# Kernel optimization log

Measured on AMD Instinct MI355X. Metric: run time of the kernel, lower is better.

Reference implementation:

```python
import jax, jax.numpy as jnp
import numpy as np

N = 100000   # nodes
E = 1600000  # directed edges (avg degree 16)
H = 64       # MODEL_HIDDEN_CHANNELS


def setup_inputs() -> dict:
    key = jax.random.key(0)
    ks = jax.random.split(key, 6)
    x = jax.random.normal(ks[0], (N, 1), dtype=jnp.float32)
    edge_index = jax.random.randint(ks[1], (2, E), 0, N, dtype=jnp.int32)
    w1 = jax.random.normal(ks[2], (1, H), dtype=jnp.float32) * 0.5
    b1 = jnp.zeros((H,), dtype=jnp.float32)
    w2 = jax.random.normal(ks[3], (H, H), dtype=jnp.float32) * (1.0 / np.sqrt(H))
    b2 = jnp.zeros((H,), dtype=jnp.float32)
    wfc = jax.random.normal(ks[4], (H, 1), dtype=jnp.float32) * (1.0 / np.sqrt(H))
    bfc = jnp.zeros((1,), dtype=jnp.float32)
    return {"x": x, "edge_index": edge_index, "w1": w1, "b1": b1,
            "w2": w2, "b2": b2, "wfc": wfc, "bfc": bfc}


def _gcn_conv(x, src, dst, norm, W, b, n):
    # PyG GCNConv: h = x @ W, then scatter-add of norm-weighted messages at dst, + bias
    h = x @ W                                   # [n, out]
    msg = h[src] * norm[:, None]                # gather + scale, [e, out]
    agg = jax.ops.segment_sum(msg, dst, num_segments=n)
    return agg + b


def reference(x, edge_index, w1, b1, w2, b2, wfc, bfc):
    n = x.shape[0]
    # add self-loops (PyG GCNConv default)
    loops = jnp.arange(n, dtype=edge_index.dtype)
    src = jnp.concatenate([edge_index[0], loops])
    dst = jnp.concatenate([edge_index[1], loops])
    # symmetric degree normalization D^{-1/2} A_hat D^{-1/2}
    deg = jax.ops.segment_sum(jnp.ones(src.shape[0], dtype=x.dtype), dst, num_segments=n)
    dinv = jnp.where(deg > 0, jax.lax.rsqrt(deg), 0.0)
    norm = dinv[src] * dinv[dst]
    h = jax.nn.relu(_gcn_conv(x, src, dst, norm, w1, b1, n))
    h = jax.nn.relu(_gcn_conv(h, src, dst, norm, w2, b2, n))
    out = h @ wfc + bfc                         # [n, 1]
    return out.reshape(-1)
```

## Files before the change

kernel.cpp:

```cpp
#include <hip/hip_runtime.h>


#define HCH 64
#define CHUNK 4096
#define BSH 7
#define BSZ 128
#define NBMAX 1024

__device__ __forceinline__ void lds_addf(float* p, float v) {
    __hip_atomic_fetch_add(p, v, __ATOMIC_RELAXED, __HIP_MEMORY_SCOPE_WORKGROUP);
}

__global__ __launch_bounds__(512) void k_init(int nb, int cap,
                                              int* __restrict__ cursor,
                                              int* __restrict__ ov_cursor,
                                              const float* __restrict__ w1,
                                              const float* __restrict__ b1,
                                              const float* __restrict__ w2,
                                              float* __restrict__ P) {
    __shared__ float part[8][4][HCH];
    __shared__ float sPo[4 * HCH];
    __shared__ float fsum;
    int t = threadIdx.x;
    for (int i = t; i < nb; i += 512) cursor[i] = i * cap;
    if (t == 0) { *ov_cursor = 0; fsum = 0.f; }
    int j = t & 63, seg = t >> 6;
    float pp = 0.f, pm = 0.f, bp = 0.f, bm = 0.f;
#pragma unroll
    for (int kk = 0; kk < 8; kk++) {
        int k = seg * 8 + kk;
        float w = w1[k], b = b1[k], v = w2[k * HCH + j];
        if (w > 0.f) { pp += w * v; bp += b * v; }
        else if (w < 0.f) { pm += w * v; bm += b * v; }
        else { float rb = b > 0.f ? b : 0.f; bp += rb * v; bm += rb * v; }
    }
    part[seg][0][j] = pp; part[seg][1][j] = pm;
    part[seg][2][j] = bp; part[seg][3][j] = bm;
    __syncthreads();
    if (t < 4 * HCH) {
        int c = t >> 6, jj = t & 63;
        float s = 0.f;
#pragma unroll
        for (int g = 0; g < 8; g++) s += part[g][c][jj];
        sPo[t] = s;
        P[t] = s;
        if (c >= 2) lds_addf(&fsum, fabsf(s));
    }
    __syncthreads();
    if (t == 0) P[4 * HCH] = fsum;
}

__global__ __launch_bounds__(512) void k_place(const int* __restrict__ src,
                                               const int* __restrict__ dst, int e,
                                               int nb, int cap,
                                               int* __restrict__ cursor,
                                               int* __restrict__ ov_cursor,
                                               int* __restrict__ packed,
                                               int2* __restrict__ ovbuf) {
    __shared__ int h[NBMAX];
    __shared__ int basel[NBMAX];
    __shared__ int avail[NBMAX];
    __shared__ int lpv[CHUNK];
    __shared__ short lb[CHUNK];
    int t = threadIdx.x;
    for (int i = t; i < nb; i += 512) h[i] = 0;
    __syncthreads();
    int cbase = blockIdx.x * CHUNK;
    int rem = min(e - cbase, CHUNK);
#pragma unroll
    for (int g = 0; g < 2; g++) {
        int li = t * 8 + g * 4;
        if (li + 3 < rem) {
            int4 s4 = *(const int4*)(src + cbase + li);
            int4 d4 = *(const int4*)(dst + cbase + li);
#pragma unroll
            for (int q = 0; q < 4; q++) {
                int sv = (q == 0) ? s4.x : (q == 1) ? s4.y : (q == 2) ? s4.z : s4.w;
                int dv = (q == 0) ? d4.x : (q == 1) ? d4.y : (q == 2) ? d4.z : d4.w;
                int b = dv >> BSH;
                atomicAdd(&h[b], 1);
                lpv[li + q] = sv | ((dv & (BSZ - 1)) << 17);
                lb[li + q] = (short)b;
            }
        } else {
            for (int q = li; q < rem && q < li + 4; q++) {
                int sv = src[cbase + q], dv = dst[cbase + q];
                int b = dv >> BSH;
                atomicAdd(&h[b], 1);
                lpv[q] = sv | ((dv & (BSZ - 1)) << 17);
                lb[q] = (short)b;
            }
        }
    }
    __syncthreads();
    for (int i = t; i < nb; i += 512) {
        int my = h[i];
        int av = 0, base = 0;
        if (my) {
            base = atomicAdd(&cursor[i], my);
            int room = (i + 1) * cap - base;
            av = room < 0 ? 0 : (room > my ? my : room);
        }
        basel[i] = base;
        avail[i] = av;
        h[i] = 0;
    }
    __syncthreads();
    for (int li = t * 8; li < t * 8 + 8 && li < rem; li++) {
        int b = lb[li];
        int pv = lpv[li];
        int loc = atomicAdd(&h[b], 1);
        if (loc < avail[b]) {
            packed[basel[b] + loc] = pv;
        } else {
            int op = atomicAdd(ov_cursor, 1);
            ovbuf[op] = make_int2(pv & 0x1FFFF, (b << BSH) | (pv >> 17));
        }
    }
}

__global__ __launch_bounds__(512) void k_bdeg(const int* __restrict__ packed,
                                              const int* __restrict__ cursor,
                                              const int* __restrict__ ov_cursor,
                                              const int2* __restrict__ ovbuf,
                                              int cap, const float* __restrict__ x, int n,
                                              float* __restrict__ dinv,
                                              float* __restrict__ y) {
    __shared__ int cnt[BSZ];
    int bk = blockIdx.x, t = threadIdx.x;
    int bbase = bk * cap;
    int bcnt = min(cursor[bk] - bbase, cap);
    if (t < BSZ) cnt[t] = 0;
    __syncthreads();
    for (int base = 0; base < bcnt; base += 2048) {
        int i0 = base + t * 4;
        if (i0 + 3 < bcnt) {
            int4 p = *(const int4*)(packed + bbase + i0);
            atomicAdd(&cnt[p.x >> 17], 1);
            atomicAdd(&cnt[p.y >> 17], 1);
            atomicAdd(&cnt[p.z >> 17], 1);
            atomicAdd(&cnt[p.w >> 17], 1);
        } else {
            for (int i = i0; i < bcnt && i < i0 + 4; i++)
                atomicAdd(&cnt[packed[bbase + i] >> 17], 1);
        }
    }
    int ovc = *ov_cursor;
    for (int i = t; i < ovc; i += 512) {
        int2 o = ovbuf[i];
        if ((o.y >> BSH) == bk) atomicAdd(&cnt[o.y & (BSZ - 1)], 1);
    }
    __syncthreads();
    int node = (bk << BSH) + t;
    if (t < BSZ && node < n) {
        float dv = rsqrtf((float)(cnt[t] + 1));
        dinv[node] = dv;
        y[node] = dv * x[node];
    }
}

__global__ __launch_bounds__(512) void k_bagg1(const int* __restrict__ packed,
                                               const int* __restrict__ cursor,
                                               const int* __restrict__ ov_cursor,
                                               const int2* __restrict__ ovbuf,
                                               int cap, const float* __restrict__ x,
                                               const float* __restrict__ dinv,
                                               const float* __restrict__ y, int n,
                                               float2* __restrict__ val2) {
    __shared__ float acc[BSZ];
    int bk = blockIdx.x, t = threadIdx.x;
    int bbase = bk * cap;
    int bcnt = min(cursor[bk] - bbase, cap);
    if (t < BSZ) acc[t] = 0.f;
    __syncthreads();
    for (int base = 0; base < bcnt; base += 2048) {
        int i0 = base + t * 4;
        if (i0 + 3 < bcnt) {
            int4 p = *(const int4*)(packed + bbase + i0);
            float y0 = y[p.x & 0x1FFFF], y1 = y[p.y & 0x1FFFF];
            float y2 = y[p.z & 0x1FFFF], y3 = y[p.w & 0x1FFFF];
            lds_addf(&acc[p.x >> 17], y0);
            lds_addf(&acc[p.y >> 17], y1);
            lds_addf(&acc[p.z >> 17], y2);
            lds_addf(&acc[p.w >> 17], y3);
        } else {
            for (int i = i0; i < bcnt && i < i0 + 4; i++) {
                int p = packed[bbase + i];
                lds_addf(&acc[p >> 17], y[p & 0x1FFFF]);
            }
        }
    }
    int ovc = *ov_cursor;
    for (int i = t; i < ovc; i += 512) {
        int2 o = ovbuf[i];
        if ((o.y >> BSH) == bk) lds_addf(&acc[o.y & (BSZ - 1)], y[o.x]);
    }
    __syncthreads();
    int node = (bk << BSH) + t;
    if (t < BSZ && node < n) {
        float dv = dinv[node];
        float s = dv * (acc[t] + dv * x[node]);
        val2[node] = make_float2(dv * s, dv);
    }
}

__global__ __launch_bounds__(512) void k_bagg2(const int* __restrict__ packed,
                                               const int* __restrict__ cursor,
                                               const int* __restrict__ ov_cursor,
                                               const int2* __restrict__ ovbuf,
                                               int cap, const float2* __restrict__ val2,
                                               const float* __restrict__ dinv,
                                               const float* __restrict__ P,
                                               const float* __restrict__ b2,
                                               const float* __restrict__ wfc,
                                               const float* __restrict__ bfc,
                                               float* __restrict__ out, int n) {
    __shared__ float aa[2 * BSZ];
    __shared__ float cc[2 * BSZ];
    __shared__ float sP[4 * HCH], sb2[HCH], swfc[HCH];
    __shared__ float sflag;
    int bk = blockIdx.x, t = threadIdx.x;
    int bbase = bk * cap;
    int bcnt = min(cursor[bk] - bbase, cap);
    if (t < 2 * BSZ) { aa[t] = 0.f; cc[t] = 0.f; }
    if (t < 4 * HCH) sP[t] = P[t];
    if (t >= 256 && t < 320) sb2[t - 256] = b2[t - 256];
    if (t >= 320 && t < 384) swfc[t - 320] = wfc[t - 320];
    if (t == 448) sflag = P[4 * HCH];
    __syncthreads();
    bool useB = sflag != 0.f;
    for (int base = 0; base < bcnt; base += 2048) {
        int i0 = base + t * 4;
        if (i0 + 3 < bcnt) {
            int4 p = *(const int4*)(packed + bbase + i0);
            float2 v0 = val2[p.x & 0x1FFFF], v1 = val2[p.y & 0x1FFFF];
            float2 v2 = val2[p.z & 0x1FFFF], v3 = val2[p.w & 0x1FFFF];
            int o0 = (v0.x > 0.f ? 0 : BSZ) + (p.x >> 17);
            int o1 = (v1.x > 0.f ? 0 : BSZ) + (p.y >> 17);
            int o2 = (v2.x > 0.f ? 0 : BSZ) + (p.z >> 17);
            int o3 = (v3.x > 0.f ? 0 : BSZ) + (p.w >> 17);
            lds_addf(&aa[o0], v0.x); lds_addf(&aa[o1], v1.x);
            lds_addf(&aa[o2], v2.x); lds_addf(&aa[o3], v3.x);
            if (useB) {
                lds_addf(&cc[o0], v0.y); lds_addf(&cc[o1], v1.y);
                lds_addf(&cc[o2], v2.y); lds_addf(&cc[o3], v3.y);
            }
        } else {
            for (int i = i0; i < bcnt && i < i0 + 4; i++) {
                int p = packed[bbase + i];
                float2 v = val2[p & 0x1FFFF];
                int off = (v.x > 0.f ? 0 : BSZ) + (p >> 17);
                lds_addf(&aa[off], v.x);
                if (useB) lds_addf(&cc[off], v.y);
            }
        }
    }
    int ovc = *ov_cursor;
    for (int i = t; i < ovc; i += 512) {
        int2 o = ovbuf[i];
        if ((o.y >> BSH) == bk) {
            float2 v = val2[o.x];
            int off = (v.x > 0.f ? 0 : BSZ) + (o.y & (BSZ - 1));
            lds_addf(&aa[off], v.x);
            if (useB) lds_addf(&cc[off], v.y);
        }
    }
    __syncthreads();
    int node = (bk << BSH) + t;
    if (t >= BSZ || node >= n) return;
    float a_p = aa[t], a_m = aa[BSZ + t], c_p = cc[t], c_m = cc[BSZ + t];
    float2 sv = val2[node];
    if (sv.x > 0.f) { a_p += sv.x; c_p += sv.y; }
    else            { a_m += sv.x; c_m += sv.y; }
    float dv = dinv[node];
    float acc = 0.f;
#pragma unroll 8
    for (int j = 0; j < HCH; j++) {
        float z = dv * (a_p * sP[j] + a_m * sP[HCH + j] +
                        c_p * sP[2 * HCH + j] + c_m * sP[3 * HCH + j]) + sb2[j];
        z = z > 0.f ? z : 0.f;
        acc += z * swfc[j];
    }
    out[node] = acc + bfc[0];
}

extern "C" void kernel_launch(void* const* d_in, const int* in_sizes, int n_in,
                              void* d_out, int out_size, void* d_ws, size_t ws_size,
                              hipStream_t stream) {
    const float* x   = (const float*)d_in[0];
    const int*   ei  = (const int*)d_in[1];
    const float* w1  = (const float*)d_in[2];
    const float* b1  = (const float*)d_in[3];
    const float* w2  = (const float*)d_in[4];
    const float* b2  = (const float*)d_in[5];
    const float* wfc = (const float*)d_in[6];
    const float* bfc = (const float*)d_in[7];
    float* out = (float*)d_out;

    const int n = in_sizes[0];
    const int e = in_sizes[1] / 2;
    const int* src = ei;
    const int* dst = ei + e;

    const int nb = (n + BSZ - 1) >> BSH;
    int avg = (e + nb - 1) / nb;
    int cap = ((avg + avg / 4 + 64) + 15) & ~15;

    auto al = [](size_t v) { return (v + 255) & ~(size_t)255; };
    char* ws = (char*)d_ws;
    size_t o = 0;
    int* cursor    = (int*)(ws + o);  o = al(o + (size_t)NBMAX * 4);
    int* ov_cursor = (int*)(ws + o);  o = al(o + 256);
    float* dinv  = (float*)(ws + o);  o = al(o + (size_t)n * 4);
    float* y     = (float*)(ws + o);  o = al(o + (size_t)n * 4);
    float2* val2 = (float2*)(ws + o); o = al(o + (size_t)n * 8);
    float* P     = (float*)(ws + o);  o = al(o + (4 * HCH + 8) * 4);
    int* packed  = (int*)(ws + o);    o = al(o + (size_t)nb * cap * 4);
    int2* ovbuf  = (int2*)(ws + o);   o = al(o + (size_t)e * 8);
    (void)ws_size;

    const int nchunk = (e + CHUNK - 1) / CHUNK;

    k_init<<<1, 512, 0, stream>>>(nb, cap, cursor, ov_cursor, w1, b1, w2, P);
    k_place<<<nchunk, 512, 0, stream>>>(src, dst, e, nb, cap, cursor, ov_cursor,
                                        packed, ovbuf);
    k_bdeg<<<nb, 512, 0, stream>>>(packed, cursor, ov_cursor, ovbuf, cap, x, n, dinv, y);
    k_bagg1<<<nb, 512, 0, stream>>>(packed, cursor, ov_cursor, ovbuf, cap, x, dinv, y,
                                    n, val2);
    k_bagg2<<<nb, 512, 0, stream>>>(packed, cursor, ov_cursor, ovbuf, cap, val2, dinv,
                                    P, b2, wfc, bfc, out, n);
}
```

Baseline: 134.5 us.

## Fuse GCN pipeline into one cooperative kernel with grid syncs and larger buckets

Replaces the five separate launches (init, place, degree, aggregation 1, aggregation 2) with a single cooperative kernel that separates phases with grid-wide syncs. Cursor, overflow counter and P are zeroed by a memset, and P is computed inside the degree phase. Bucket size grows from 128 to 256 nodes, which halves the bucket count and gives each block more edges. The aim is to remove per-launch overhead and tail gaps between kernels. In exchange it adds grid.sync costs, caps the grid at what can be co-resident (391 blocks of 512 threads), and uses a larger shared-memory union that may limit occupancy.

```diff
diff --git a/kernel.cpp b/kernel.cpp
--- a/kernel.cpp
+++ b/kernel.cpp
@@ -1,274 +1,244 @@
 #include <hip/hip_runtime.h>
+#include <hip/hip_cooperative_groups.h>
+
+namespace cg = cooperative_groups;
 
 
 #define HCH 64
 #define CHUNK 4096
-#define BSH 7
-#define BSZ 128
-#define NBMAX 1024
+#define BSH 8
+#define BSZ 256
+#define NBMAX 512
 
 __device__ __forceinline__ void lds_addf(float* p, float v) {
     __hip_atomic_fetch_add(p, v, __ATOMIC_RELAXED, __HIP_MEMORY_SCOPE_WORKGROUP);
 }
 
-__global__ __launch_bounds__(512) void k_init(int nb, int cap,
-                                              int* __restrict__ cursor,
-                                              int* __restrict__ ov_cursor,
-                                              const float* __restrict__ w1,
-                                              const float* __restrict__ b1,
-                                              const float* __restrict__ w2,
-                                              float* __restrict__ P) {
-    __shared__ float part[8][4][HCH];
-    __shared__ float sPo[4 * HCH];
-    __shared__ float fsum;
+union SMem {
+    struct { int h[NBMAX]; int basel[NBMAX]; int avail[NBMAX];
+             int lpv[CHUNK]; short lb[CHUNK]; } pl;
+    struct { int cnt[BSZ]; } bd;
+    struct { float acc[BSZ]; } g1;
+    struct { float aa[2 * BSZ]; float cc[2 * BSZ];
+             float sP[4 * HCH]; float sb2[HCH]; float swfc[HCH]; } g2;
+};
+
+__global__ __launch_bounds__(512, 4) void k_fused(
+    const int* __restrict__ src, const int* __restrict__ dst, int e, int n,
+    int nb, int nchunk, int cap,
+    int* __restrict__ cursor, int* __restrict__ ov_cursor,
+    int2* __restrict__ ovbuf, int* __restrict__ packed,
+    const float* __restrict__ x, float* __restrict__ dinv,
+    float* __restrict__ y, float2* __restrict__ val2,
+    const float* __restrict__ w1, const float* __restrict__ b1,
+    const float* __restrict__ w2, float* __restrict__ P,
+    const float* __restrict__ b2v, const float* __restrict__ wfc,
+    const float* __restrict__ bfc, float* __restrict__ out) {
+    __shared__ SMem sm;
+    cg::grid_group grid = cg::this_grid();
     int t = threadIdx.x;
-    for (int i = t; i < nb; i += 512) cursor[i] = i * cap;
-    if (t == 0) { *ov_cursor = 0; fsum = 0.f; }
-    int j = t & 63, seg = t >> 6;
-    float pp = 0.f, pm = 0.f, bp = 0.f, bm = 0.f;
+    int bid = blockIdx.x;
+
+    if (bid < nchunk) {
+        for (int i = t; i < nb; i += 512) sm.pl.h[i] = 0;
+        __syncthreads();
+        int cbase = bid * CHUNK;
+        int rem = min(e - cbase, CHUNK);
 #pragma unroll
-    for (int kk = 0; kk < 8; kk++) {
-        int k = seg * 8 + kk;
-        float w = w1[k], b = b1[k], v = w2[k * HCH + j];
-        if (w > 0.f) { pp += w * v; bp += b * v; }
-        else if (w < 0.f) { pm += w * v; bm += b * v; }
-        else { float rb = b > 0.f ? b : 0.f; bp += rb * v; bm += rb * v; }
-    }
-    part[seg][0][j] = pp; part[seg][1][j] = pm;
-    part[seg][2][j] = bp; part[seg][3][j] = bm;
+        for (int g = 0; g < 2; g++) {
+            int li = t * 8 + g * 4;
+            if (li + 3 < rem) {
+                int4 s4 = *(const int4*)(src + cbase + li);
+                int4 d4 = *(const int4*)(dst + cbase + li);
+#pragma unroll
+                for (int q = 0; q < 4; q++) {
+                    int sv = (q == 0) ? s4.x : (q == 1) ? s4.y : (q == 2) ? s4.z : s4.w;
+                    int dv = (q == 0) ? d4.x : (q == 1) ? d4.y : (q == 2) ? d4.z : d4.w;
+                    int b = dv >> BSH;
+                    atomicAdd(&sm.pl.h[b], 1);
+                    sm.pl.lpv[li + q] = sv | ((dv & (BSZ - 1)) << 17);
+                    sm.pl.lb[li + q] = (short)b;
+                }
+            } else {
+                for (int q = li; q < rem && q < li + 4; q++) {
+                    int sv = src[cbase + q], dv = dst[cbase + q];
+                    int b = dv >> BSH;
+                    atomicAdd(&sm.pl.h[b], 1);
+                    sm.pl.lpv[q] = sv | ((dv & (BSZ - 1)) << 17);
+                    sm.pl.lb[q] = (short)b;
+                }
+            }
+        }
+        __syncthreads();
+        for (int i = t; i < nb; i += 512) {
+            int my = sm.pl.h[i];
+            int av = 0, base = 0;
+            if (my) {
+                base = atomicAdd(&cursor[i], my);
+                int room = cap - base;
+                av = room < 0 ? 0 : (room > my ? my : room);
+            }
+            sm.pl.basel[i] = i * cap + base;
+            sm.pl.avail[i] = av;
+            sm.pl.h[i] = 0;
+        }
+        __syncthreads();
+        int lim = min(rem, t * 8 + 8);
+        for (int li = t * 8; li < lim; li++) {
+            int b = sm.pl.lb[li];
+            int pv = sm.pl.lpv[li];
+            int loc = atomicAdd(&sm.pl.h[b], 1);
+            if (loc < sm.pl.avail[b]) {
+                packed[sm.pl.basel[b] + loc] = pv;
+            } else {
+                int op = atomicAdd(ov_cursor, 1);
+                ovbuf[op] = make_int2(pv & 0x1FFFF, (b << BSH) | (pv >> 17));
+            }
+        }
+    }
+    grid.sync();
+
+    if (bid < nb) {
+        if (t < BSZ) sm.bd.cnt[t] = 0;
+        __syncthreads();
+        int bbase = bid * cap;
+        int bcnt = min(cursor[bid], cap);
+        for (int base = 0; base < bcnt; base += 2048) {
+            int i0 = base + t * 4;
+            if (i0 + 3 < bcnt) {
+                int4 p = *(const int4*)(packed + bbase + i0);
+                atomicAdd(&sm.bd.cnt[p.x >> 17], 1);
+                atomicAdd(&sm.bd.cnt[p.y >> 17], 1);
+                atomicAdd(&sm.bd.cnt[p.z >> 17], 1);
+                atomicAdd(&sm.bd.cnt[p.w >> 17], 1);
+            } else {
+                for (int i = i0; i < bcnt && i < i0 + 4; i++)
+                    atomicAdd(&sm.bd.cnt[packed[bbase + i] >> 17], 1);
+            }
+        }
+        int ovc = *ov_cursor;
+        for (int i = t; i < ovc; i += 512) {
+            int2 o = ovbuf[i];
+            if ((o.y >> BSH) == bid) atomicAdd(&sm.bd.cnt[o.y & (BSZ - 1)], 1);
+        }
+        __syncthreads();
+        int node = (bid << BSH) + t;
+        if (t < BSZ && node < n) {
+            float dv = rsqrtf((float)(sm.bd.cnt[t] + 1));
+            dinv[node] = dv;
+            y[node] = dv * x[node];
+        }
+    }
+    if (bid == 0 && t < 4 * HCH) {
+        int c = t >> 6, j = t & 63;
+        float acc = 0.f;
+        for (int k = 0; k < HCH; k++) {
+            float w = w1[k], b = b1[k], v = w2[k * HCH + j];
+            if (c == 0)      acc += (w > 0.f) ? w * v : 0.f;
+            else if (c == 1) acc += (w < 0.f) ? w * v : 0.f;
+            else if (c == 2) acc += (w > 0.f) ? b * v : (w == 0.f ? fmaxf(b, 0.f) * v : 0.f);
+            else             acc += (w < 0.f) ? b * v : (w == 0.f ? fmaxf(b, 0.f) * v : 0.f);
+        }
+        P[t] = acc;
+        if (c >= 2) {
+            float f = fabsf(acc);
+#pragma unroll
+            for (int off = 32; off; off >>= 1) f += __shfl_xor(f, off, 64);
+            if ((t & 63) == 0) atomicAdd(&P[4 * HCH], f);
+        }
+    }
+    grid.sync();
+
+    if (bid < nb) {
+        if (t < BSZ) sm.g1.acc[t] = 0.f;
+        __syncthreads();
+        int bbase = bid * cap;
+        int bcnt = min(cursor[bid], cap);
+        for (int base = 0; base < bcnt; base += 2048) {
+            int i0 = base + t * 4;
+            if (i0 + 3 < bcnt) {
+                int4 p = *(const int4*)(packed + bbase + i0);
+                float y0 = y[p.x & 0x1FFFF], y1 = y[p.y & 0x1FFFF];
+                float y2 = y[p.z & 0x1FFFF], y3 = y[p.w & 0x1FFFF];
+                lds_addf(&sm.g1.acc[p.x >> 17], y0);
+                lds_addf(&sm.g1.acc[p.y >> 17], y1);
+                lds_addf(&sm.g1.acc[p.z >> 17], y2);
+                lds_addf(&sm.g1.acc[p.w >> 17], y3);
+            } else {
+                for (int i = i0; i < bcnt && i < i0 + 4; i++) {
+                    int p = packed[bbase + i];
+                    lds_addf(&sm.g1.acc[p >> 17], y[p & 0x1FFFF]);
+                }
+            }
+        }
+        int ovc = *ov_cursor;
+        for (int i = t; i < ovc; i += 512) {
+            int2 o = ovbuf[i];
+            if ((o.y >> BSH) == bid) lds_addf(&sm.g1.acc[o.y & (BSZ - 1)], y[o.x]);
+        }
+        __syncthreads();
+        int node = (bid << BSH) + t;
+        if (t < BSZ && node < n) {
+            float dv = dinv[node];
+            float s = dv * (sm.g1.acc[t] + dv * x[node]);
+            val2[node] = make_float2(dv * s, dv);
+        }
+    }
+    grid.sync();
+
+    if (bid >= nb) return;
+    sm.g2.aa[t] = 0.f;
+    sm.g2.cc[t] = 0.f;
+    if (t < 4 * HCH) sm.g2.sP[t] = P[t];
+    if (t >= 256 && t < 320) sm.g2.sb2[t - 256] = b2v[t - 256];
+    if (t >= 320 && t < 384) sm.g2.swfc[t - 320] = wfc[t - 320];
     __syncthreads();
-    if (t < 4 * HCH) {
-        int c = t >> 6, jj = t & 63;
-        float s = 0.f;
-#pragma unroll
-        for (int g = 0; g < 8; g++) s += part[g][c][jj];
-        sPo[t] = s;
-        P[t] = s;
-        if (c >= 2) lds_addf(&fsum, fabsf(s));
+    bool useB = P[4 * HCH] != 0.f;
+    {
+        int bbase = bid * cap;
+        int bcnt = min(cursor[bid], cap);
+        for (int base = 0; base < bcnt; base += 2048) {
+            int i0 = base + t * 4;
+            if (i0 + 3 < bcnt) {
+                int4 p = *(const int4*)(packed + bbase + i0);
+                float2 v0 = val2[p.x & 0x1FFFF], v1 = val2[p.y & 0x1FFFF];
+                float2 v2 = val2[p.z & 0x1FFFF], v3 = val2[p.w & 0x1FFFF];
+                int o0 = (v0.x > 0.f ? 0 : BSZ) + (p.x >> 17);
+                int o1 = (v1.x > 0.f ? 0 : BSZ) + (p.y >> 17);
+                int o2 = (v2.x > 0.f ? 0 : BSZ) + (p.z >> 17);
+                int o3 = (v3.x > 0.f ? 0 : BSZ) + (p.w >> 17);
+                lds_addf(&sm.g2.aa[o0], v0.x); lds_addf(&sm.g2.aa[o1], v1.x);
+                lds_addf(&sm.g2.aa[o2], v2.x); lds_addf(&sm.g2.aa[o3], v3.x);
+                if (useB) {
+                    lds_addf(&sm.g2.cc[o0], v0.y); lds_addf(&sm.g2.cc[o1], v1.y);
+                    lds_addf(&sm.g2.cc[o2], v2.y); lds_addf(&sm.g2.cc[o3], v3.y);
+                }
+            } else {
+                for (int i = i0; i < bcnt && i < i0 + 4; i++) {
+                    int p = packed[bbase + i];
+                    float2 v = val2[p & 0x1FFFF];
+                    int off = (v.x > 0.f ? 0 : BSZ) + (p >> 17);
+                    lds_addf(&sm.g2.aa[off], v.x);
+                    if (useB) lds_addf(&sm.g2.cc[off], v.y);
+                }
+            }
+        }
+        int ovc = *ov_cursor;
+        for (int i = t; i < ovc; i += 512) {
+            int2 o = ovbuf[i];
+            if ((o.y >> BSH) == bid) {
+                float2 v = val2[o.x];
+                int off = (v.x > 0.f ? 0 : BSZ) + (o.y & (BSZ - 1));
+                lds_addf(&sm.g2.aa[off], v.x);
+                if (useB) lds_addf(&sm.g2.cc[off], v.y);
+            }
+        }
     }
     __syncthreads();
-    if (t == 0) P[4 * HCH] = fsum;
-}
-
-__global__ __launch_bounds__(512) void k_place(const int* __restrict__ src,
-                                               const int* __restrict__ dst, int e,
-                                               int nb, int cap,
-                                               int* __restrict__ cursor,
-                                               int* __restrict__ ov_cursor,
-                                               int* __restrict__ packed,
-                                               int2* __restrict__ ovbuf) {
-    __shared__ int h[NBMAX];
-    __shared__ int basel[NBMAX];
-    __shared__ int avail[NBMAX];
-    __shared__ int lpv[CHUNK];
-    __shared__ short lb[CHUNK];
-    int t = threadIdx.x;
-    for (int i = t; i < nb; i += 512) h[i] = 0;
-    __syncthreads();
-    int cbase = blockIdx.x * CHUNK;
-    int rem = min(e - cbase, CHUNK);
-#pragma unroll
-    for (int g = 0; g < 2; g++) {
-        int li = t * 8 + g * 4;
-        if (li + 3 < rem) {
-            int4 s4 = *(const int4*)(src + cbase + li);
-            int4 d4 = *(const int4*)(dst + cbase + li);
-#pragma unroll
-            for (int q = 0; q < 4; q++) {
-                int sv = (q == 0) ? s4.x : (q == 1) ? s4.y : (q == 2) ? s4.z : s4.w;
-                int dv = (q == 0) ? d4.x : (q == 1) ? d4.y : (q == 2) ? d4.z : d4.w;
-                int b = dv >> BSH;
-                atomicAdd(&h[b], 1);
-                lpv[li + q] = sv | ((dv & (BSZ - 1)) << 17);
-                lb[li + q] = (short)b;
-            }
-        } else {
-            for (int q = li; q < rem && q < li + 4; q++) {
-                int sv = src[cbase + q], dv = dst[cbase + q];
-                int b = dv >> BSH;
-                atomicAdd(&h[b], 1);
-                lpv[q] = sv | ((dv & (BSZ - 1)) << 17);
-                lb[q] = (short)b;
-            }
-        }
-    }
-    __syncthreads();
-    for (int i = t; i < nb; i += 512) {
-        int my = h[i];
-        int av = 0, base = 0;
-        if (my) {
-            base = atomicAdd(&cursor[i], my);
-            int room = (i + 1) * cap - base;
-            av = room < 0 ? 0 : (room > my ? my : room);
-        }
-        basel[i] = base;
-        avail[i] = av;
-        h[i] = 0;
-    }
-    __syncthreads();
-    for (int li = t * 8; li < t * 8 + 8 && li < rem; li++) {
-        int b = lb[li];
-        int pv = lpv[li];
-        int loc = atomicAdd(&h[b], 1);
-        if (loc < avail[b]) {
-            packed[basel[b] + loc] = pv;
-        } else {
-            int op = atomicAdd(ov_cursor, 1);
-            ovbuf[op] = make_int2(pv & 0x1FFFF, (b << BSH) | (pv >> 17));
-        }
-    }
-}
-
-__global__ __launch_bounds__(512) void k_bdeg(const int* __restrict__ packed,
-                                              const int* __restrict__ cursor,
-                                              const int* __restrict__ ov_cursor,
-                                              const int2* __restrict__ ovbuf,
-                                              int cap, const float* __restrict__ x, int n,
-                                              float* __restrict__ dinv,
-                                              float* __restrict__ y) {
-    __shared__ int cnt[BSZ];
-    int bk = blockIdx.x, t = threadIdx.x;
-    int bbase = bk * cap;
-    int bcnt = min(cursor[bk] - bbase, cap);
-    if (t < BSZ) cnt[t] = 0;
-    __syncthreads();
-    for (int base = 0; base < bcnt; base += 2048) {
-        int i0 = base + t * 4;
-        if (i0 + 3 < bcnt) {
-            int4 p = *(const int4*)(packed + bbase + i0);
-            atomicAdd(&cnt[p.x >> 17], 1);
-            atomicAdd(&cnt[p.y >> 17], 1);
-            atomicAdd(&cnt[p.z >> 17], 1);
-            atomicAdd(&cnt[p.w >> 17], 1);
-        } else {
-            for (int i = i0; i < bcnt && i < i0 + 4; i++)
-                atomicAdd(&cnt[packed[bbase + i] >> 17], 1);
-        }
-    }
-    int ovc = *ov_cursor;
-    for (int i = t; i < ovc; i += 512) {
-        int2 o = ovbuf[i];
-        if ((o.y >> BSH) == bk) atomicAdd(&cnt[o.y & (BSZ - 1)], 1);
-    }
-    __syncthreads();
-    int node = (bk << BSH) + t;
-    if (t < BSZ && node < n) {
-        float dv = rsqrtf((float)(cnt[t] + 1));
-        dinv[node] = dv;
-        y[node] = dv * x[node];
-    }
-}
-
-__global__ __launch_bounds__(512) void k_bagg1(const int* __restrict__ packed,
-                                               const int* __restrict__ cursor,
-                                               const int* __restrict__ ov_cursor,
-                                               const int2* __restrict__ ovbuf,
-                                               int cap, const float* __restrict__ x,
-                                               const float* __restrict__ dinv,
-                                               const float* __restrict__ y, int n,
-                                               float2* __restrict__ val2) {
-    __shared__ float acc[BSZ];
-    int bk = blockIdx.x, t = threadIdx.x;
-    int bbase = bk * cap;
-    int bcnt = min(cursor[bk] - bbase, cap);
-    if (t < BSZ) acc[t] = 0.f;
-    __syncthreads();
-    for (int base = 0; base < bcnt; base += 2048) {
-        int i0 = base + t * 4;
-        if (i0 + 3 < bcnt) {
-            int4 p = *(const int4*)(packed + bbase + i0);
-            float y0 = y[p.x & 0x1FFFF], y1 = y[p.y & 0x1FFFF];
-            float y2 = y[p.z & 0x1FFFF], y3 = y[p.w & 0x1FFFF];
-            lds_addf(&acc[p.x >> 17], y0);
-            lds_addf(&acc[p.y >> 17], y1);
-            lds_addf(&acc[p.z >> 17], y2);
-            lds_addf(&acc[p.w >> 17], y3);
-        } else {
-            for (int i = i0; i < bcnt && i < i0 + 4; i++) {
-                int p = packed[bbase + i];
-                lds_addf(&acc[p >> 17], y[p & 0x1FFFF]);
-            }
-        }
-    }
-    int ovc = *ov_cursor;
-    for (int i = t; i < ovc; i += 512) {
-        int2 o = ovbuf[i];
-        if ((o.y >> BSH) == bk) lds_addf(&acc[o.y & (BSZ - 1)], y[o.x]);
-    }
-    __syncthreads();
-    int node = (bk << BSH) + t;
-    if (t < BSZ && node < n) {
-        float dv = dinv[node];
-        float s = dv * (acc[t] + dv * x[node]);
-        val2[node] = make_float2(dv * s, dv);
-    }
-}
-
-__global__ __launch_bounds__(512) void k_bagg2(const int* __restrict__ packed,
-                                               const int* __restrict__ cursor,
-                                               const int* __restrict__ ov_cursor,
-                                               const int2* __restrict__ ovbuf,
-                                               int cap, const float2* __restrict__ val2,
-                                               const float* __restrict__ dinv,
-                                               const float* __restrict__ P,
-                                               const float* __restrict__ b2,
-                                               const float* __restrict__ wfc,
-                                               const float* __restrict__ bfc,
-                                               float* __restrict__ out, int n) {
-    __shared__ float aa[2 * BSZ];
-    __shared__ float cc[2 * BSZ];
-    __shared__ float sP[4 * HCH], sb2[HCH], swfc[HCH];
-    __shared__ float sflag;
-    int bk = blockIdx.x, t = threadIdx.x;
-    int bbase = bk * cap;
-    int bcnt = min(cursor[bk] - bbase, cap);
-    if (t < 2 * BSZ) { aa[t] = 0.f; cc[t] = 0.f; }
-    if (t < 4 * HCH) sP[t] = P[t];
-    if (t >= 256 && t < 320) sb2[t - 256] = b2[t - 256];
-    if (t >= 320 && t < 384) swfc[t - 320] = wfc[t - 320];
-    if (t == 448) sflag = P[4 * HCH];
-    __syncthreads();
-    bool useB = sflag != 0.f;
-    for (int base = 0; base < bcnt; base += 2048) {
-        int i0 = base + t * 4;
-        if (i0 + 3 < bcnt) {
-            int4 p = *(const int4*)(packed + bbase + i0);
-            float2 v0 = val2[p.x & 0x1FFFF], v1 = val2[p.y & 0x1FFFF];
-            float2 v2 = val2[p.z & 0x1FFFF], v3 = val2[p.w & 0x1FFFF];
-            int o0 = (v0.x > 0.f ? 0 : BSZ) + (p.x >> 17);
-            int o1 = (v1.x > 0.f ? 0 : BSZ) + (p.y >> 17);
-            int o2 = (v2.x > 0.f ? 0 : BSZ) + (p.z >> 17);
-            int o3 = (v3.x > 0.f ? 0 : BSZ) + (p.w >> 17);
-            lds_addf(&aa[o0], v0.x); lds_addf(&aa[o1], v1.x);
-            lds_addf(&aa[o2], v2.x); lds_addf(&aa[o3], v3.x);
-            if (useB) {
-                lds_addf(&cc[o0], v0.y); lds_addf(&cc[o1], v1.y);
-                lds_addf(&cc[o2], v2.y); lds_addf(&cc[o3], v3.y);
-            }
-        } else {
-            for (int i = i0; i < bcnt && i < i0 + 4; i++) {
-                int p = packed[bbase + i];
-                float2 v = val2[p & 0x1FFFF];
-                int off = (v.x > 0.f ? 0 : BSZ) + (p >> 17);
-                lds_addf(&aa[off], v.x);
-                if (useB) lds_addf(&cc[off], v.y);
-            }
-        }
-    }
-    int ovc = *ov_cursor;
-    for (int i = t; i < ovc; i += 512) {
-        int2 o = ovbuf[i];
-        if ((o.y >> BSH) == bk) {
-            float2 v = val2[o.x];
-            int off = (v.x > 0.f ? 0 : BSZ) + (o.y & (BSZ - 1));
-            lds_addf(&aa[off], v.x);
-            if (useB) lds_addf(&cc[off], v.y);
-        }
-    }
-    __syncthreads();
-    int node = (bk << BSH) + t;
+    int node = (bid << BSH) + t;
     if (t >= BSZ || node >= n) return;
-    float a_p = aa[t], a_m = aa[BSZ + t], c_p = cc[t], c_m = cc[BSZ + t];
+    float a_p = sm.g2.aa[t], a_m = sm.g2.aa[BSZ + t];
+    float c_p = sm.g2.cc[t], c_m = sm.g2.cc[BSZ + t];
     float2 sv = val2[node];
     if (sv.x > 0.f) { a_p += sv.x; c_p += sv.y; }
     else            { a_m += sv.x; c_m += sv.y; }
@@ -276,10 +246,11 @@
     float acc = 0.f;
 #pragma unroll 8
     for (int j = 0; j < HCH; j++) {
-        float z = dv * (a_p * sP[j] + a_m * sP[HCH + j] +
-                        c_p * sP[2 * HCH + j] + c_m * sP[3 * HCH + j]) + sb2[j];
-        z = z > 0.f ? z : 0.f;
-        acc += z * swfc[j];
+        float z = dv * (a_p * sm.g2.sP[j] + a_m * sm.g2.sP[HCH + j] +
+                        c_p * sm.g2.sP[2 * HCH + j] + c_m * sm.g2.sP[3 * HCH + j]) +
+                  sm.g2.sb2[j];
+        z = fmaxf(z, 0.f);
+        acc += z * sm.g2.swfc[j];
     }
     out[node] = acc + bfc[0];
 }
@@ -297,36 +268,37 @@
     const float* bfc = (const float*)d_in[7];
     float* out = (float*)d_out;
 
-    const int n = in_sizes[0];
-    const int e = in_sizes[1] / 2;
+    int n = in_sizes[0];
+    int e = in_sizes[1] / 2;
     const int* src = ei;
     const int* dst = ei + e;
 
-    const int nb = (n + BSZ - 1) >> BSH;
+    int nb = (n + BSZ - 1) >> BSH;
+    int nchunk = (e + CHUNK - 1) / CHUNK;
     int avg = (e + nb - 1) / nb;
     int cap = ((avg + avg / 4 + 64) + 15) & ~15;
 
     auto al = [](size_t v) { return (v + 255) & ~(size_t)255; };
     char* ws = (char*)d_ws;
     size_t o = 0;
-    int* cursor    = (int*)(ws + o);  o = al(o + (size_t)NBMAX * 4);
-    int* ov_cursor = (int*)(ws + o);  o = al(o + 256);
+    int* cursor    = (int*)(ws + o);  o += (size_t)NBMAX * 4;
+    int* ov_cursor = (int*)(ws + o);  o += 256;
+    float* P       = (float*)(ws + o); o += (4 * HCH + 8) * 4;
+    size_t zbytes = o;
+    o = al(o);
     float* dinv  = (float*)(ws + o);  o = al(o + (size_t)n * 4);
     float* y     = (float*)(ws + o);  o = al(o + (size_t)n * 4);
     float2* val2 = (float2*)(ws + o); o = al(o + (size_t)n * 8);
-    float* P     = (float*)(ws + o);  o = al(o + (4 * HCH + 8) * 4);
     int* packed  = (int*)(ws + o);    o = al(o + (size_t)nb * cap * 4);
     int2* ovbuf  = (int2*)(ws + o);   o = al(o + (size_t)e * 8);
     (void)ws_size;
 
-    const int nchunk = (e + CHUNK - 1) / CHUNK;
-
-    k_init<<<1, 512, 0, stream>>>(nb, cap, cursor, ov_cursor, w1, b1, w2, P);
-    k_place<<<nchunk, 512, 0, stream>>>(src, dst, e, nb, cap, cursor, ov_cursor,
-                                        packed, ovbuf);
-    k_bdeg<<<nb, 512, 0, stream>>>(packed, cursor, ov_cursor, ovbuf, cap, x, n, dinv, y);
-    k_bagg1<<<nb, 512, 0, stream>>>(packed, cursor, ov_cursor, ovbuf, cap, x, dinv, y,
-                                    n, val2);
-    k_bagg2<<<nb, 512, 0, stream>>>(packed, cursor, ov_cursor, ovbuf, cap, val2, dinv,
-                                    P, b2, wfc, bfc, out, n);
+    int grid = nb > nchunk ? nb : nchunk;
+
+    hipMemsetAsync(ws, 0, zbytes, stream);
+    void* args[] = {&src, &dst, &e, &n, &nb, &nchunk, &cap,
+                    &cursor, &ov_cursor, &ovbuf, &packed,
+                    &x, &dinv, &y, &val2,
+                    &w1, &b1, &w2, &P, &b2, &wfc, &bfc, &out};
+    hipLaunchCooperativeKernel((void*)k_fused, dim3(grid), dim3(512), args, 0, stream);
 }
```

New measurement: 313.1 us. 2.33x slower.

## Drop init kernel: memset cursors, fold weight precompute into degree kernel

Applied to the files above, without the earlier changes.

Removes the single-block init kernel. Cursors, the overflow counter and P are now zeroed with one hipMemsetAsync, and cursors hold offsets relative to each bucket instead of absolute positions. The W1·W2 split precompute moves into block 0 of the degree kernel, which uses a wave shuffle reduction and a global atomic for the bias-magnitude flag. The placement kernel also switches to 1024 threads with 4 edges per thread. Together these remove one dependent launch from the chain, at the cost of a memset node and extra serial work in one block of k_bdeg.

```diff
diff --git a/kernel.cpp b/kernel.cpp
--- a/kernel.cpp
+++ b/kernel.cpp
@@ -11,104 +11,63 @@
     __hip_atomic_fetch_add(p, v, __ATOMIC_RELAXED, __HIP_MEMORY_SCOPE_WORKGROUP);
 }
 
-__global__ __launch_bounds__(512) void k_init(int nb, int cap,
-                                              int* __restrict__ cursor,
-                                              int* __restrict__ ov_cursor,
-                                              const float* __restrict__ w1,
-                                              const float* __restrict__ b1,
-                                              const float* __restrict__ w2,
-                                              float* __restrict__ P) {
-    __shared__ float part[8][4][HCH];
-    __shared__ float sPo[4 * HCH];
-    __shared__ float fsum;
-    int t = threadIdx.x;
-    for (int i = t; i < nb; i += 512) cursor[i] = i * cap;
-    if (t == 0) { *ov_cursor = 0; fsum = 0.f; }
-    int j = t & 63, seg = t >> 6;
-    float pp = 0.f, pm = 0.f, bp = 0.f, bm = 0.f;
-#pragma unroll
-    for (int kk = 0; kk < 8; kk++) {
-        int k = seg * 8 + kk;
-        float w = w1[k], b = b1[k], v = w2[k * HCH + j];
-        if (w > 0.f) { pp += w * v; bp += b * v; }
-        else if (w < 0.f) { pm += w * v; bm += b * v; }
-        else { float rb = b > 0.f ? b : 0.f; bp += rb * v; bm += rb * v; }
-    }
-    part[seg][0][j] = pp; part[seg][1][j] = pm;
-    part[seg][2][j] = bp; part[seg][3][j] = bm;
-    __syncthreads();
-    if (t < 4 * HCH) {
-        int c = t >> 6, jj = t & 63;
-        float s = 0.f;
-#pragma unroll
-        for (int g = 0; g < 8; g++) s += part[g][c][jj];
-        sPo[t] = s;
-        P[t] = s;
-        if (c >= 2) lds_addf(&fsum, fabsf(s));
-    }
-    __syncthreads();
-    if (t == 0) P[4 * HCH] = fsum;
-}
-
-__global__ __launch_bounds__(512) void k_place(const int* __restrict__ src,
-                                               const int* __restrict__ dst, int e,
-                                               int nb, int cap,
-                                               int* __restrict__ cursor,
-                                               int* __restrict__ ov_cursor,
-                                               int* __restrict__ packed,
-                                               int2* __restrict__ ovbuf) {
+__global__ __launch_bounds__(1024) void k_place(const int* __restrict__ src,
+                                                const int* __restrict__ dst, int e,
+                                                int nb, int cap,
+                                                int* __restrict__ cursor,
+                                                int* __restrict__ ov_cursor,
+                                                int* __restrict__ packed,
+                                                int2* __restrict__ ovbuf) {
     __shared__ int h[NBMAX];
     __shared__ int basel[NBMAX];
     __shared__ int avail[NBMAX];
     __shared__ int lpv[CHUNK];
     __shared__ short lb[CHUNK];
     int t = threadIdx.x;
-    for (int i = t; i < nb; i += 512) h[i] = 0;
+    if (t < nb) h[t] = 0;
     __syncthreads();
     int cbase = blockIdx.x * CHUNK;
     int rem = min(e - cbase, CHUNK);
+    int li = t * 4;
+    if (li + 3 < rem) {
+        int4 s4 = *(const int4*)(src + cbase + li);
+        int4 d4 = *(const int4*)(dst + cbase + li);
 #pragma unroll
-    for (int g = 0; g < 2; g++) {
-        int li = t * 8 + g * 4;
-        if (li + 3 < rem) {
-            int4 s4 = *(const int4*)(src + cbase + li);
-            int4 d4 = *(const int4*)(dst + cbase + li);
-#pragma unroll
-            for (int q = 0; q < 4; q++) {
-                int sv = (q == 0) ? s4.x : (q == 1) ? s4.y : (q == 2) ? s4.z : s4.w;
-                int dv = (q == 0) ? d4.x : (q == 1) ? d4.y : (q == 2) ? d4.z : d4.w;
-                int b = dv >> BSH;
-                atomicAdd(&h[b], 1);
-                lpv[li + q] = sv | ((dv & (BSZ - 1)) << 17);
-                lb[li + q] = (short)b;
-            }
-        } else {
-            for (int q = li; q < rem && q < li + 4; q++) {
-                int sv = src[cbase + q], dv = dst[cbase + q];
-                int b = dv >> BSH;
-                atomicAdd(&h[b], 1);
-                lpv[q] = sv | ((dv & (BSZ - 1)) << 17);
-                lb[q] = (short)b;
-            }
-        }
-    }
-    __syncthreads();
-    for (int i = t; i < nb; i += 512) {
-        int my = h[i];
+        for (int q = 0; q < 4; q++) {
+            int sv = (q == 0) ? s4.x : (q == 1) ? s4.y : (q == 2) ? s4.z : s4.w;
+            int dv = (q == 0) ? d4.x : (q == 1) ? d4.y : (q == 2) ? d4.z : d4.w;
+            int b = dv >> BSH;
+            atomicAdd(&h[b], 1);
+            lpv[li + q] = sv | ((dv & (BSZ - 1)) << 17);
+            lb[li + q] = (short)b;
+        }
+    } else {
+        for (int q = li; q < rem && q < li + 4; q++) {
+            int sv = src[cbase + q], dv = dst[cbase + q];
+            int b = dv >> BSH;
+            atomicAdd(&h[b], 1);
+            lpv[q] = sv | ((dv & (BSZ - 1)) << 17);
+            lb[q] = (short)b;
+        }
+    }
+    __syncthreads();
+    if (t < nb) {
+        int my = h[t];
         int av = 0, base = 0;
         if (my) {
-            base = atomicAdd(&cursor[i], my);
-            int room = (i + 1) * cap - base;
+            base = atomicAdd(&cursor[t], my);
+            int room = cap - base;
             av = room < 0 ? 0 : (room > my ? my : room);
         }
-        basel[i] = base;
-        avail[i] = av;
-        h[i] = 0;
-    }
-    __syncthreads();
-    for (int li = t * 8; li < t * 8 + 8 && li < rem; li++) {
-        int b = lb[li];
-        int pv = lpv[li];
+        basel[t] = t * cap + base;
+        avail[t] = av;
+        h[t] = 0;
+    }
+    __syncthreads();
+    int lim = min(rem, li + 4);
+    for (int q = li; q < lim; q++) {
+        int b = lb[q];
+        int pv = lpv[q];
         int loc = atomicAdd(&h[b], 1);
         if (loc < avail[b]) {
             packed[basel[b] + loc] = pv;
@@ -125,11 +84,15 @@
                                               const int2* __restrict__ ovbuf,
                                               int cap, const float* __restrict__ x, int n,
                                               float* __restrict__ dinv,
-                                              float* __restrict__ y) {
+                                              float* __restrict__ y,
+                                              const float* __restrict__ w1,
+                                              const float* __restrict__ b1,
+                                              const float* __restrict__ w2,
+                                              float* __restrict__ P) {
     __shared__ int cnt[BSZ];
     int bk = blockIdx.x, t = threadIdx.x;
     int bbase = bk * cap;
-    int bcnt = min(cursor[bk] - bbase, cap);
+    int bcnt = min(cursor[bk], cap);
     if (t < BSZ) cnt[t] = 0;
     __syncthreads();
     for (int base = 0; base < bcnt; base += 2048) {
@@ -157,6 +120,25 @@
         dinv[node] = dv;
         y[node] = dv * x[node];
     }
+    if (bk == 0 && t >= 128 && t < 384) {
+        int tt = t - 128;
+        int c = tt >> 6, j = tt & 63;
+        float acc = 0.f;
+        for (int k = 0; k < HCH; k++) {
+            float w = w1[k], b = b1[k], v = w2[k * HCH + j];
+            if (c == 0)      acc += (w > 0.f) ? w * v : 0.f;
+            else if (c == 1) acc += (w < 0.f) ? w * v : 0.f;
+            else if (c == 2) acc += (w > 0.f) ? b * v : (w == 0.f ? fmaxf(b, 0.f) * v : 0.f);
+            else             acc += (w < 0.f) ? b * v : (w == 0.f ? fmaxf(b, 0.f) * v : 0.f);
+        }
+        P[c * HCH + j] = acc;
+        if (c >= 2) {
+            float f = fabsf(acc);
+#pragma unroll
+            for (int off = 32; off; off >>= 1) f += __shfl_xor(f, off, 64);
+            if ((t & 63) == 0) atomicAdd(&P[4 * HCH], f);
+        }
+    }
 }
 
 __global__ __launch_bounds__(512) void k_bagg1(const int* __restrict__ packed,
@@ -170,7 +152,7 @@
     __shared__ float acc[BSZ];
     int bk = blockIdx.x, t = threadIdx.x;
     int bbase = bk * cap;
-    int bcnt = min(cursor[bk] - bbase, cap);
+    int bcnt = min(cursor[bk], cap);
     if (t < BSZ) acc[t] = 0.f;
     __syncthreads();
     for (int base = 0; base < bcnt; base += 2048) {
@@ -218,17 +200,15 @@
     __shared__ float aa[2 * BSZ];
     __shared__ float cc[2 * BSZ];
     __shared__ float sP[4 * HCH], sb2[HCH], swfc[HCH];
-    __shared__ float sflag;
     int bk = blockIdx.x, t = threadIdx.x;
     int bbase = bk * cap;
-    int bcnt = min(cursor[bk] - bbase, cap);
+    int bcnt = min(cursor[bk], cap);
     if (t < 2 * BSZ) { aa[t] = 0.f; cc[t] = 0.f; }
     if (t < 4 * HCH) sP[t] = P[t];
     if (t >= 256 && t < 320) sb2[t - 256] = b2[t - 256];
     if (t >= 320 && t < 384) swfc[t - 320] = wfc[t - 320];
-    if (t == 448) sflag = P[4 * HCH];
-    __syncthreads();
-    bool useB = sflag != 0.f;
+    __syncthreads();
+    bool useB = P[4 * HCH] != 0.f;
     for (int base = 0; base < bcnt; base += 2048) {
         int i0 = base + t * 4;
         if (i0 + 3 < bcnt) {
@@ -278,7 +258,7 @@
     for (int j = 0; j < HCH; j++) {
         float z = dv * (a_p * sP[j] + a_m * sP[HCH + j] +
                         c_p * sP[2 * HCH + j] + c_m * sP[3 * HCH + j]) + sb2[j];
-        z = z > 0.f ? z : 0.f;
+        z = fmaxf(z, 0.f);
         acc += z * swfc[j];
     }
     out[node] = acc + bfc[0];
@@ -309,22 +289,25 @@
     auto al = [](size_t v) { return (v + 255) & ~(size_t)255; };
     char* ws = (char*)d_ws;
     size_t o = 0;
-    int* cursor    = (int*)(ws + o);  o = al(o + (size_t)NBMAX * 4);
-    int* ov_cursor = (int*)(ws + o);  o = al(o + 256);
+    int* cursor    = (int*)(ws + o);  o += (size_t)NBMAX * 4;
+    int* ov_cursor = (int*)(ws + o);  o += 256;
+    float* P       = (float*)(ws + o); o += (4 * HCH + 8) * 4;
+    size_t zbytes = o;
+    o = al(o);
     float* dinv  = (float*)(ws + o);  o = al(o + (size_t)n * 4);
     float* y     = (float*)(ws + o);  o = al(o + (size_t)n * 4);
     float2* val2 = (float2*)(ws + o); o = al(o + (size_t)n * 8);
-    float* P     = (float*)(ws + o);  o = al(o + (4 * HCH + 8) * 4);
     int* packed  = (int*)(ws + o);    o = al(o + (size_t)nb * cap * 4);
     int2* ovbuf  = (int2*)(ws + o);   o = al(o + (size_t)e * 8);
     (void)ws_size;
 
     const int nchunk = (e + CHUNK - 1) / CHUNK;
 
-    k_init<<<1, 512, 0, stream>>>(nb, cap, cursor, ov_cursor, w1, b1, w2, P);
-    k_place<<<nchunk, 512, 0, stream>>>(src, dst, e, nb, cap, cursor, ov_cursor,
-                                        packed, ovbuf);
-    k_bdeg<<<nb, 512, 0, stream>>>(packed, cursor, ov_cursor, ovbuf, cap, x, n, dinv, y);
+    hipMemsetAsync(ws, 0, zbytes, stream);
+    k_place<<<nchunk, 1024, 0, stream>>>(src, dst, e, nb, cap, cursor, ov_cursor,
+                                         packed, ovbuf);
+    k_bdeg<<<nb, 512, 0, stream>>>(packed, cursor, ov_cursor, ovbuf, cap, x, n,
+                                   dinv, y, w1, b1, w2, P);
     k_bagg1<<<nb, 512, 0, stream>>>(packed, cursor, ov_cursor, ovbuf, cap, x, dinv, y,
                                     n, val2);
     k_bagg2<<<nb, 512, 0, stream>>>(packed, cursor, ov_cursor, ovbuf, cap, val2, dinv,
```

After: 139.7 us. 1.04x slower.
